# Performance work log

Measured on AMD Instinct MI355X. Metric: run time of the kernel, lower is better.

## Reference

```python
import jax, jax.numpy as jnp
import numpy as np

N_NODES = 100000
N_EDGES = 1600000
IN_CH = 64
HEADS = 8
OUT_CH = 16
NEG_SLOPE = 0.2  # PyG GATConv default


def setup_inputs() -> dict:
    key = jax.random.key(0)
    ks = jax.random.split(key, 6)
    x = jax.random.normal(ks[0], (N_NODES, IN_CH), dtype=jnp.float32)
    edge_index = jax.random.randint(ks[1], (2, N_EDGES), 0, N_NODES, dtype=jnp.int32)
    # learned parameters (PyG GATConv: shared lin for src/dst, att vectors, bias for concat output)
    W = jax.random.normal(ks[2], (HEADS * OUT_CH, IN_CH), dtype=jnp.float32) / np.sqrt(IN_CH)
    att_src = jax.random.normal(ks[3], (HEADS, OUT_CH), dtype=jnp.float32) / np.sqrt(OUT_CH)
    att_dst = jax.random.normal(ks[4], (HEADS, OUT_CH), dtype=jnp.float32) / np.sqrt(OUT_CH)
    bias = jax.random.normal(ks[5], (HEADS * OUT_CH,), dtype=jnp.float32) * 0.01
    return {"x": x, "edge_index": edge_index, "W": W,
            "att_src": att_src, "att_dst": att_dst, "bias": bias}


def reference(x, edge_index, W, att_src, att_dst, bias):
    n = x.shape[0]
    # linear projection -> [N, H, C]
    h = (x @ W.T).reshape(n, HEADS, OUT_CH)
    # per-node halves of the attention logit
    a_src = jnp.einsum('nhc,hc->nh', h, att_src)  # [N, H]
    a_dst = jnp.einsum('nhc,hc->nh', h, att_dst)  # [N, H]
    # add self loops (PyG default add_self_loops=True)
    loops = jnp.arange(n, dtype=edge_index.dtype)
    src = jnp.concatenate([edge_index[0], loops])
    dst = jnp.concatenate([edge_index[1], loops])
    # edge attention: leaky_relu then segment-softmax over incoming edges of dst
    e = jax.nn.leaky_relu(a_src[src] + a_dst[dst], NEG_SLOPE)  # [E+N, H]
    e_max = jax.ops.segment_max(e, dst, num_segments=n)
    e = jnp.exp(e - e_max[dst])
    denom = jax.ops.segment_sum(e, dst, num_segments=n)
    alpha = e / (denom[dst] + 1e-16)  # [E+N, H]
    # weighted scatter-add aggregation
    msg = h[src] * alpha[:, :, None]  # [E+N, H, C]
    out = jax.ops.segment_sum(msg, dst, num_segments=n).reshape(n, HEADS * OUT_CH)
    out = out + bias
    # unlinear: act='relu', norm=None
    return jax.nn.relu(out)
```

## Files before the change

kernel.cpp:

```cpp
#include <hip/hip_runtime.h>

#define N_NODESC 100000
#define N_EDGESC 1600000
#define HCC 128
#define E_TOTC (N_EDGESC + N_NODESC)
#define SCAN_NB 391
#define PROJ_NB 782

__device__ __forceinline__ float lrelu(float v) { return fmaxf(v, 0.2f * v); }
__device__ __forceinline__ unsigned short f2bf(float f) {
    unsigned u = __float_as_uint(f);
    unsigned r = ((u >> 16) & 1u) + 0x7fffu;
    return (unsigned short)((u + r) >> 16);
}

__global__ void wu_kernel(const float* __restrict__ W,
                          const float* __restrict__ att_src, const float* __restrict__ att_dst,
                          float* __restrict__ WT, float* __restrict__ us_g) {
    int t = blockIdx.x * 256 + threadIdx.x;
    if (t < 8192) {
        int k = t >> 7, c = t & 127;
        WT[t] = W[c * 64 + k];
    } else {
        int o = t - 8192;
        int k = o >> 4, c = o & 15;
        const int h = (c < 8) ? c : c - 8;
        const float* av = (c < 8) ? att_src : att_dst;
        float s = 0.f;
#pragma unroll
        for (int j = 0; j < 16; ++j) s += av[h * 16 + j] * W[(h * 16 + j) * 64 + k];
        us_g[o] = s;
    }
}

__launch_bounds__(256, 2)
__global__ void proj_kernel(const float* __restrict__ x, const float* __restrict__ WT,
                            const float* __restrict__ us_g,
                            unsigned short* __restrict__ h16,
                            float* __restrict__ a_src, float* __restrict__ a_dst) {
    __shared__ float xs[128][68];
    __shared__ float ws[64][132];
    __shared__ float us[64][16];
    const int t = threadIdx.x;
    const int row0 = blockIdx.x * 128;

    const float4* wt4 = (const float4*)WT;
    float4* ws4 = (float4*)&ws[0][0];
#pragma unroll
    for (int j = 0; j < 8; ++j) {
        int q = t + 256 * j;
        int k = q >> 5, c4 = q & 31;
        *(float4*)&ws[k][c4 * 4] = wt4[q];
    }
    ((float4*)&us[0][0])[t] = ((const float4*)us_g)[t];

#pragma unroll
    for (int j = 0; j < 8; ++j) {
        int f = (t + 256 * j) * 4;
        int r = f >> 6, k = f & 63;
        int gr = row0 + r;
        if (gr >= N_NODESC) gr = N_NODESC - 1;
        float4 v = *(const float4*)&x[(size_t)gr * 64 + k];
        *(float4*)&xs[r][k] = v;
    }
    __syncthreads();

    const int rg = t & 15;
    const int cg = t >> 4;
    float acc[8][8], acca[8];
#pragma unroll
    for (int i = 0; i < 8; ++i) {
        acca[i] = 0.f;
#pragma unroll
        for (int j = 0; j < 8; ++j) acc[i][j] = 0.f;
    }

#pragma unroll 4
    for (int k = 0; k < 64; ++k) {
        float xv[8];
#pragma unroll
        for (int i = 0; i < 8; ++i) xv[i] = xs[rg + 16 * i][k];
        float4 w0 = *(const float4*)&ws[k][4 * cg];
        float4 w1 = *(const float4*)&ws[k][64 + 4 * cg];
        float uv = us[k][cg];
#pragma unroll
        for (int i = 0; i < 8; ++i) {
            acc[i][0] += xv[i] * w0.x; acc[i][1] += xv[i] * w0.y;
            acc[i][2] += xv[i] * w0.z; acc[i][3] += xv[i] * w0.w;
            acc[i][4] += xv[i] * w1.x; acc[i][5] += xv[i] * w1.y;
            acc[i][6] += xv[i] * w1.z; acc[i][7] += xv[i] * w1.w;
            acca[i]   += xv[i] * uv;
        }
    }

#pragma unroll
    for (int i = 0; i < 8; ++i) {
        int gr = row0 + rg + 16 * i;
        if (gr < N_NODESC) {
            ushort4 p0, p1;
            p0.x = f2bf(acc[i][0]); p0.y = f2bf(acc[i][1]); p0.z = f2bf(acc[i][2]); p0.w = f2bf(acc[i][3]);
            p1.x = f2bf(acc[i][4]); p1.y = f2bf(acc[i][5]); p1.z = f2bf(acc[i][6]); p1.w = f2bf(acc[i][7]);
            *(ushort4*)&h16[(size_t)gr * HCC + 4 * cg] = p0;
            *(ushort4*)&h16[(size_t)gr * HCC + 64 + 4 * cg] = p1;
            if (cg < 8) a_src[(size_t)gr * 8 + cg] = acca[i];
            else        a_dst[(size_t)gr * 8 + cg - 8] = acca[i];
        }
    }
}

__global__ void pos_kernel(const int* __restrict__ ei, int* __restrict__ deg,
                           int* __restrict__ posb) {
    int e = blockIdx.x * 256 + threadIdx.x;
    if (e >= E_TOTC) return;
    int d = (e < N_EDGESC) ? ei[N_EDGESC + e] : (e - N_EDGESC);
    posb[e] = atomicAdd(&deg[d], 1);
}

__global__ void scan1_kernel(const int* __restrict__ deg, int* __restrict__ bsum) {
    __shared__ int lds[256];
    int i = blockIdx.x * 256 + threadIdx.x;
    lds[threadIdx.x] = (i < N_NODESC) ? deg[i] : 0;
    __syncthreads();
    for (int off = 128; off > 0; off >>= 1) {
        if (threadIdx.x < off) lds[threadIdx.x] += lds[threadIdx.x + off];
        __syncthreads();
    }
    if (threadIdx.x == 0) bsum[blockIdx.x] = lds[0];
}

__global__ void scan2_kernel(int* __restrict__ bsum) {
    __shared__ int lds[512];
    int t = threadIdx.x;
    lds[t] = (t < SCAN_NB) ? bsum[t] : 0;
    __syncthreads();
    for (int off = 1; off < 512; off <<= 1) {
        int u = 0;
        if (t >= off) u = lds[t - off];
        __syncthreads();
        if (t >= off) lds[t] += u;
        __syncthreads();
    }
    if (t < SCAN_NB) bsum[t] = (t == 0) ? 0 : lds[t - 1];
}

__global__ void scan3_kernel(const int* __restrict__ deg, const int* __restrict__ bsum,
                             int* __restrict__ rowptr) {
    __shared__ int lds[256];
    int t = threadIdx.x;
    int i = blockIdx.x * 256 + t;
    int v = (i < N_NODESC) ? deg[i] : 0;
    lds[t] = v;
    __syncthreads();
    for (int off = 1; off < 256; off <<= 1) {
        int u = 0;
        if (t >= off) u = lds[t - off];
        __syncthreads();
        if (t >= off) lds[t] += u;
        __syncthreads();
    }
    int excl = bsum[blockIdx.x] + lds[t] - v;
    if (i < N_NODESC) rowptr[i] = excl;
    if (i == 0) rowptr[N_NODESC] = E_TOTC;
}

__global__ void scatter_kernel(const int* __restrict__ ei, const int* __restrict__ rowptr,
                               const int* __restrict__ posb, int* __restrict__ colsrc) {
    int e = blockIdx.x * 256 + threadIdx.x;
    if (e >= E_TOTC) return;
    int s, d;
    if (e < N_EDGESC) { s = ei[e]; d = ei[N_EDGESC + e]; }
    else              { s = d = e - N_EDGESC; }
    colsrc[rowptr[d] + posb[e]] = s;
}

__launch_bounds__(256, 8)
__global__ void agg_csr_kernel(const int* __restrict__ rowptr, const int* __restrict__ colsrc,
                               const float* __restrict__ a_src, const float* __restrict__ a_dst,
                               const unsigned* __restrict__ h32,
                               const float* __restrict__ bias, float* __restrict__ out) {
    const int t = threadIdx.x;
    const int L = t & 63;
    const int n = blockIdx.x * 4 + (t >> 6);
    const int hd = L >> 3;
    const int eL = L & 7;

    const int beg = rowptr[n], end = rowptr[n + 1];
    const float ad = a_dst[n * 8 + hd];

    float den = 0.f;
    float acc[16];
#pragma unroll
    for (int j = 0; j < 16; ++j) acc[j] = 0.f;

    int p = beg + eL;
    bool vld = p < end;
    int s = vld ? colsrc[p] : 0;
    float av = vld ? a_src[s * 8 + hd] : 0.f;

    while (vld) {
        const uint4* hp = (const uint4*)(h32 + (size_t)s * 64 + hd * 8);
        const uint4 ha = hp[0];
        const uint4 hb = hp[1];
        const int p2 = p + 8;
        const bool v2 = p2 < end;
        const int s2 = v2 ? colsrc[p2] : 0;
        const float av2 = v2 ? a_src[s2 * 8 + hd] : 0.f;

        const float pr = __expf(lrelu(av + ad));
        den += pr;
        acc[0]  = fmaf(pr, __uint_as_float(ha.x << 16),         acc[0]);
        acc[1]  = fmaf(pr, __uint_as_float(ha.x & 0xffff0000u), acc[1]);
        acc[2]  = fmaf(pr, __uint_as_float(ha.y << 16),         acc[2]);
        acc[3]  = fmaf(pr, __uint_as_float(ha.y & 0xffff0000u), acc[3]);
        acc[4]  = fmaf(pr, __uint_as_float(ha.z << 16),         acc[4]);
        acc[5]  = fmaf(pr, __uint_as_float(ha.z & 0xffff0000u), acc[5]);
        acc[6]  = fmaf(pr, __uint_as_float(ha.w << 16),         acc[6]);
        acc[7]  = fmaf(pr, __uint_as_float(ha.w & 0xffff0000u), acc[7]);
        acc[8]  = fmaf(pr, __uint_as_float(hb.x << 16),         acc[8]);
        acc[9]  = fmaf(pr, __uint_as_float(hb.x & 0xffff0000u), acc[9]);
        acc[10] = fmaf(pr, __uint_as_float(hb.y << 16),         acc[10]);
        acc[11] = fmaf(pr, __uint_as_float(hb.y & 0xffff0000u), acc[11]);
        acc[12] = fmaf(pr, __uint_as_float(hb.z << 16),         acc[12]);
        acc[13] = fmaf(pr, __uint_as_float(hb.z & 0xffff0000u), acc[13]);
        acc[14] = fmaf(pr, __uint_as_float(hb.w << 16),         acc[14]);
        acc[15] = fmaf(pr, __uint_as_float(hb.w & 0xffff0000u), acc[15]);

        p = p2; s = s2; av = av2; vld = v2;
    }

    den += __shfl_xor(den, 1); den += __shfl_xor(den, 2); den += __shfl_xor(den, 4);
#pragma unroll
    for (int j = 0; j < 16; ++j) {
        acc[j] += __shfl_xor(acc[j], 1);
        acc[j] += __shfl_xor(acc[j], 2);
        acc[j] += __shfl_xor(acc[j], 4);
    }
    const float inv = 1.f / (den + 1e-16f);
    float ox = acc[0], oy = acc[1];
#pragma unroll
    for (int j = 1; j < 8; ++j) {
        ox = (eL == j) ? acc[2 * j]     : ox;
        oy = (eL == j) ? acc[2 * j + 1] : oy;
    }
    const float2 b = ((const float2*)bias)[L];
    float2 o;
    o.x = fmaxf(ox * inv + b.x, 0.f);
    o.y = fmaxf(oy * inv + b.y, 0.f);
    ((float2*)out)[(size_t)n * 64 + L] = o;
}

extern "C" void kernel_launch(void* const* d_in, const int* in_sizes, int n_in,
                              void* d_out, int out_size, void* d_ws, size_t ws_size,
                              hipStream_t stream) {
    const float* x       = (const float*)d_in[0];
    const int*   ei      = (const int*)d_in[1];
    const float* W       = (const float*)d_in[2];
    const float* att_src = (const float*)d_in[3];
    const float* att_dst = (const float*)d_in[4];
    const float* bias    = (const float*)d_in[5];
    float* out = (float*)d_out;

    float* ws    = (float*)d_ws;
    unsigned short* h16 = (unsigned short*)ws;
    float* a_src = ws + 6400000;
    float* a_dst = a_src + 800000;
    float* WT    = a_dst + 800000;
    float* us_g  = WT + 8192;
    int* deg     = (int*)(us_g + 1024);
    int* rowptr  = deg + 100000;
    int* bsum    = rowptr + 100001;
    int* posb    = bsum + 512;
    int* colsrc  = posb + 1700000;

    hipMemsetAsync(deg, 0, 100000 * sizeof(int), stream);

    wu_kernel<<<36, 256, 0, stream>>>(W, att_src, att_dst, WT, us_g);
    proj_kernel<<<PROJ_NB, 256, 0, stream>>>(x, WT, us_g, h16, a_src, a_dst);
    pos_kernel<<<(E_TOTC + 255) / 256, 256, 0, stream>>>(ei, deg, posb);
    scan1_kernel<<<SCAN_NB, 256, 0, stream>>>(deg, bsum);
    scan2_kernel<<<1, 512, 0, stream>>>(bsum);
    scan3_kernel<<<SCAN_NB, 256, 0, stream>>>(deg, bsum, rowptr);
    scatter_kernel<<<(E_TOTC + 255) / 256, 256, 0, stream>>>(ei, rowptr, posb, colsrc);

    agg_csr_kernel<<<N_NODESC / 4, 256, 0, stream>>>(rowptr, colsrc, a_src, a_dst,
                                                     (const unsigned*)h16, bias, out);
}
```

Measured before the change: 230.2 us.

## Fuse setup kernels, use single-pass decoupled-lookback scan, persistent aggregation

Merges the weight-transpose kernel with the degree/position atomic kernel, collapses the three-kernel scan into one decoupled-lookback scan with flag-tagged block states, and turns the CSR aggregation into a persistent kernel that pulls four nodes at a time from an atomic counter and prefetches their first neighbours. The aim is to cut launch count and inter-kernel bubbles and to improve load balance and latency hiding in the gather. The lookback scan relies on blocks making forward progress in order, and the persistent loop adds atomic-counter contention.

```diff
diff --git a/kernel.cpp b/kernel.cpp
--- a/kernel.cpp
+++ b/kernel.cpp
@@ -6,6 +6,12 @@
 #define E_TOTC (N_EDGESC + N_NODESC)
 #define SCAN_NB 391
 #define PROJ_NB 782
+#define POS_NB 6641
+#define WU_NB 36
+
+#define FLAG_AGG 0x40000000u
+#define FLAG_PRE 0x80000000u
+#define VAL_MASK 0x3fffffffu
 
 __device__ __forceinline__ float lrelu(float v) { return fmaxf(v, 0.2f * v); }
 __device__ __forceinline__ unsigned short f2bf(float f) {
@@ -14,23 +20,32 @@
     return (unsigned short)((u + r) >> 16);
 }
 
-__global__ void wu_kernel(const float* __restrict__ W,
-                          const float* __restrict__ att_src, const float* __restrict__ att_dst,
-                          float* __restrict__ WT, float* __restrict__ us_g) {
-    int t = blockIdx.x * 256 + threadIdx.x;
-    if (t < 8192) {
-        int k = t >> 7, c = t & 127;
-        WT[t] = W[c * 64 + k];
-    } else {
-        int o = t - 8192;
-        int k = o >> 4, c = o & 15;
-        const int h = (c < 8) ? c : c - 8;
-        const float* av = (c < 8) ? att_src : att_dst;
-        float s = 0.f;
-#pragma unroll
-        for (int j = 0; j < 16; ++j) s += av[h * 16 + j] * W[(h * 16 + j) * 64 + k];
-        us_g[o] = s;
-    }
+__global__ void wu_pos_kernel(const float* __restrict__ W,
+                              const float* __restrict__ att_src, const float* __restrict__ att_dst,
+                              float* __restrict__ WT, float* __restrict__ us_g,
+                              const int* __restrict__ ei, int* __restrict__ deg,
+                              int* __restrict__ posb) {
+    if (blockIdx.x < WU_NB) {
+        int t = blockIdx.x * 256 + threadIdx.x;
+        if (t < 8192) {
+            int k = t >> 7, c = t & 127;
+            WT[t] = W[c * 64 + k];
+        } else if (t < 9216) {
+            int o = t - 8192;
+            int k = o >> 4, c = o & 15;
+            const int h = (c < 8) ? c : c - 8;
+            const float* av = (c < 8) ? att_src : att_dst;
+            float s = 0.f;
+#pragma unroll
+            for (int j = 0; j < 16; ++j) s += av[h * 16 + j] * W[(h * 16 + j) * 64 + k];
+            us_g[o] = s;
+        }
+        return;
+    }
+    int e = (blockIdx.x - WU_NB) * 256 + threadIdx.x;
+    if (e >= E_TOTC) return;
+    int d = (e < N_EDGESC) ? ei[N_EDGESC + e] : (e - N_EDGESC);
+    posb[e] = atomicAdd(&deg[d], 1);
 }
 
 __launch_bounds__(256, 2)
@@ -45,7 +60,6 @@
     const int row0 = blockIdx.x * 128;
 
     const float4* wt4 = (const float4*)WT;
-    float4* ws4 = (float4*)&ws[0][0];
 #pragma unroll
     for (int j = 0; j < 8; ++j) {
         int q = t + 256 * j;
@@ -108,47 +122,13 @@
     }
 }
 
-__global__ void pos_kernel(const int* __restrict__ ei, int* __restrict__ deg,
-                           int* __restrict__ posb) {
-    int e = blockIdx.x * 256 + threadIdx.x;
-    if (e >= E_TOTC) return;
-    int d = (e < N_EDGESC) ? ei[N_EDGESC + e] : (e - N_EDGESC);
-    posb[e] = atomicAdd(&deg[d], 1);
-}
-
-__global__ void scan1_kernel(const int* __restrict__ deg, int* __restrict__ bsum) {
+__global__ void scan_kernel(const int* __restrict__ deg, unsigned* __restrict__ state,
+                            int* __restrict__ rowptr) {
     __shared__ int lds[256];
-    int i = blockIdx.x * 256 + threadIdx.x;
-    lds[threadIdx.x] = (i < N_NODESC) ? deg[i] : 0;
-    __syncthreads();
-    for (int off = 128; off > 0; off >>= 1) {
-        if (threadIdx.x < off) lds[threadIdx.x] += lds[threadIdx.x + off];
-        __syncthreads();
-    }
-    if (threadIdx.x == 0) bsum[blockIdx.x] = lds[0];
-}
-
-__global__ void scan2_kernel(int* __restrict__ bsum) {
-    __shared__ int lds[512];
-    int t = threadIdx.x;
-    lds[t] = (t < SCAN_NB) ? bsum[t] : 0;
-    __syncthreads();
-    for (int off = 1; off < 512; off <<= 1) {
-        int u = 0;
-        if (t >= off) u = lds[t - off];
-        __syncthreads();
-        if (t >= off) lds[t] += u;
-        __syncthreads();
-    }
-    if (t < SCAN_NB) bsum[t] = (t == 0) ? 0 : lds[t - 1];
-}
-
-__global__ void scan3_kernel(const int* __restrict__ deg, const int* __restrict__ bsum,
-                             int* __restrict__ rowptr) {
-    __shared__ int lds[256];
-    int t = threadIdx.x;
-    int i = blockIdx.x * 256 + t;
-    int v = (i < N_NODESC) ? deg[i] : 0;
+    __shared__ int s_prefix;
+    const int b = blockIdx.x, t = threadIdx.x;
+    const int i = b * 256 + t;
+    const int v = (i < N_NODESC) ? deg[i] : 0;
     lds[t] = v;
     __syncthreads();
     for (int off = 1; off < 256; off <<= 1) {
@@ -158,9 +138,28 @@
         if (t >= off) lds[t] += u;
         __syncthreads();
     }
-    int excl = bsum[blockIdx.x] + lds[t] - v;
-    if (i < N_NODESC) rowptr[i] = excl;
-    if (i == 0) rowptr[N_NODESC] = E_TOTC;
+    const int incl = lds[t];
+    const int total = lds[255];
+    if (t == 0) {
+        if (b == 0) {
+            atomicExch(&state[0], FLAG_PRE | (unsigned)total);
+            s_prefix = 0;
+        } else {
+            atomicExch(&state[b], FLAG_AGG | (unsigned)total);
+            unsigned run = 0;
+            int j = b - 1;
+            while (true) {
+                unsigned s = atomicAdd(&state[j], 0u);
+                if (s & FLAG_PRE) { run += s & VAL_MASK; break; }
+                if (s & FLAG_AGG) { run += s & VAL_MASK; --j; }
+            }
+            atomicExch(&state[b], FLAG_PRE | ((unsigned)total + run));
+            s_prefix = (int)run;
+        }
+    }
+    __syncthreads();
+    const int excl = s_prefix + incl - v;
+    if (i <= N_NODESC) rowptr[i] = excl;
 }
 
 __global__ void scatter_kernel(const int* __restrict__ ei, const int* __restrict__ rowptr,
@@ -174,79 +173,105 @@
 }
 
 __launch_bounds__(256, 8)
-__global__ void agg_csr_kernel(const int* __restrict__ rowptr, const int* __restrict__ colsrc,
-                               const float* __restrict__ a_src, const float* __restrict__ a_dst,
-                               const unsigned* __restrict__ h32,
-                               const float* __restrict__ bias, float* __restrict__ out) {
+__global__ void agg_pers_kernel(const int* __restrict__ rowptr, const int* __restrict__ colsrc,
+                                const float* __restrict__ a_src, const float* __restrict__ a_dst,
+                                const unsigned* __restrict__ h32,
+                                const float* __restrict__ bias, float* __restrict__ out,
+                                int* __restrict__ ctr) {
     const int t = threadIdx.x;
     const int L = t & 63;
-    const int n = blockIdx.x * 4 + (t >> 6);
     const int hd = L >> 3;
     const int eL = L & 7;
-
-    const int beg = rowptr[n], end = rowptr[n + 1];
-    const float ad = a_dst[n * 8 + hd];
-
-    float den = 0.f;
-    float acc[16];
-#pragma unroll
-    for (int j = 0; j < 16; ++j) acc[j] = 0.f;
-
-    int p = beg + eL;
-    bool vld = p < end;
-    int s = vld ? colsrc[p] : 0;
-    float av = vld ? a_src[s * 8 + hd] : 0.f;
-
-    while (vld) {
-        const uint4* hp = (const uint4*)(h32 + (size_t)s * 64 + hd * 8);
-        const uint4 ha = hp[0];
-        const uint4 hb = hp[1];
-        const int p2 = p + 8;
-        const bool v2 = p2 < end;
-        const int s2 = v2 ? colsrc[p2] : 0;
-        const float av2 = v2 ? a_src[s2 * 8 + hd] : 0.f;
-
-        const float pr = __expf(lrelu(av + ad));
-        den += pr;
-        acc[0]  = fmaf(pr, __uint_as_float(ha.x << 16),         acc[0]);
-        acc[1]  = fmaf(pr, __uint_as_float(ha.x & 0xffff0000u), acc[1]);
-        acc[2]  = fmaf(pr, __uint_as_float(ha.y << 16),         acc[2]);
-        acc[3]  = fmaf(pr, __uint_as_float(ha.y & 0xffff0000u), acc[3]);
-        acc[4]  = fmaf(pr, __uint_as_float(ha.z << 16),         acc[4]);
-        acc[5]  = fmaf(pr, __uint_as_float(ha.z & 0xffff0000u), acc[5]);
-        acc[6]  = fmaf(pr, __uint_as_float(ha.w << 16),         acc[6]);
-        acc[7]  = fmaf(pr, __uint_as_float(ha.w & 0xffff0000u), acc[7]);
-        acc[8]  = fmaf(pr, __uint_as_float(hb.x << 16),         acc[8]);
-        acc[9]  = fmaf(pr, __uint_as_float(hb.x & 0xffff0000u), acc[9]);
-        acc[10] = fmaf(pr, __uint_as_float(hb.y << 16),         acc[10]);
-        acc[11] = fmaf(pr, __uint_as_float(hb.y & 0xffff0000u), acc[11]);
-        acc[12] = fmaf(pr, __uint_as_float(hb.z << 16),         acc[12]);
-        acc[13] = fmaf(pr, __uint_as_float(hb.z & 0xffff0000u), acc[13]);
-        acc[14] = fmaf(pr, __uint_as_float(hb.w << 16),         acc[14]);
-        acc[15] = fmaf(pr, __uint_as_float(hb.w & 0xffff0000u), acc[15]);
-
-        p = p2; s = s2; av = av2; vld = v2;
-    }
-
-    den += __shfl_xor(den, 1); den += __shfl_xor(den, 2); den += __shfl_xor(den, 4);
-#pragma unroll
-    for (int j = 0; j < 16; ++j) {
-        acc[j] += __shfl_xor(acc[j], 1);
-        acc[j] += __shfl_xor(acc[j], 2);
-        acc[j] += __shfl_xor(acc[j], 4);
-    }
-    const float inv = 1.f / (den + 1e-16f);
-    float ox = acc[0], oy = acc[1];
-#pragma unroll
-    for (int j = 1; j < 8; ++j) {
-        ox = (eL == j) ? acc[2 * j]     : ox;
-        oy = (eL == j) ? acc[2 * j + 1] : oy;
-    }
-    const float2 b = ((const float2*)bias)[L];
-    float2 o;
-    o.x = fmaxf(ox * inv + b.x, 0.f);
-    o.y = fmaxf(oy * inv + b.y, 0.f);
-    ((float2*)out)[(size_t)n * 64 + L] = o;
+    const float2 b2 = ((const float2*)bias)[L];
+
+    while (true) {
+        int base = 0;
+        if (L == 0) base = atomicAdd(ctr, 4);
+        base = __shfl(base, 0);
+        if (base >= N_NODESC) return;
+
+        const int rv = rowptr[min(base + (L & 7), N_NODESC)];
+        const float adv = a_dst[min(base * 8 + L, N_NODESC * 8 - 1)];
+
+        int s0[4];
+        float av0[4];
+#pragma unroll
+        for (int j = 0; j < 4; ++j) {
+            int bj = __shfl(rv, j);
+            s0[j] = colsrc[min(bj + eL, E_TOTC - 1)];
+        }
+#pragma unroll
+        for (int j = 0; j < 4; ++j) av0[j] = a_src[s0[j] * 8 + hd];
+
+#pragma unroll
+        for (int j = 0; j < 4; ++j) {
+            const int n = base + j;
+            if (n >= N_NODESC) break;
+            const int beg = __shfl(rv, j);
+            const int end = __shfl(rv, j + 1);
+            const float ad = __shfl(adv, j * 8 + hd);
+
+            float den = 0.f;
+            float acc[16];
+#pragma unroll
+            for (int q = 0; q < 16; ++q) acc[q] = 0.f;
+
+            int p = beg + eL;
+            bool vld = p < end;
+            int s = s0[j];
+            float av = av0[j];
+
+            while (vld) {
+                const uint4* hp = (const uint4*)(h32 + (size_t)s * 64 + hd * 8);
+                const uint4 ha = hp[0];
+                const uint4 hb = hp[1];
+                const int p2 = p + 8;
+                const bool v2 = p2 < end;
+                const int s2 = v2 ? colsrc[p2] : 0;
+                const float av2 = v2 ? a_src[s2 * 8 + hd] : 0.f;
+
+                const float pr = __expf(lrelu(av + ad));
+                den += pr;
+                acc[0]  = fmaf(pr, __uint_as_float(ha.x << 16),         acc[0]);
+                acc[1]  = fmaf(pr, __uint_as_float(ha.x & 0xffff0000u), acc[1]);
+                acc[2]  = fmaf(pr, __uint_as_float(ha.y << 16),         acc[2]);
+                acc[3]  = fmaf(pr, __uint_as_float(ha.y & 0xffff0000u), acc[3]);
+                acc[4]  = fmaf(pr, __uint_as_float(ha.z << 16),         acc[4]);
+                acc[5]  = fmaf(pr, __uint_as_float(ha.z & 0xffff0000u), acc[5]);
+                acc[6]  = fmaf(pr, __uint_as_float(ha.w << 16),         acc[6]);
+                acc[7]  = fmaf(pr, __uint_as_float(ha.w & 0xffff0000u), acc[7]);
+                acc[8]  = fmaf(pr, __uint_as_float(hb.x << 16),         acc[8]);
+                acc[9]  = fmaf(pr, __uint_as_float(hb.x & 0xffff0000u), acc[9]);
+                acc[10] = fmaf(pr, __uint_as_float(hb.y << 16),         acc[10]);
+                acc[11] = fmaf(pr, __uint_as_float(hb.y & 0xffff0000u), acc[11]);
+                acc[12] = fmaf(pr, __uint_as_float(hb.z << 16),         acc[12]);
+                acc[13] = fmaf(pr, __uint_as_float(hb.z & 0xffff0000u), acc[13]);
+                acc[14] = fmaf(pr, __uint_as_float(hb.w << 16),         acc[14]);
+                acc[15] = fmaf(pr, __uint_as_float(hb.w & 0xffff0000u), acc[15]);
+
+                p = p2; s = s2; av = av2; vld = v2;
+            }
+
+            den += __shfl_xor(den, 1); den += __shfl_xor(den, 2); den += __shfl_xor(den, 4);
+#pragma unroll
+            for (int q = 0; q < 16; ++q) {
+                acc[q] += __shfl_xor(acc[q], 1);
+                acc[q] += __shfl_xor(acc[q], 2);
+                acc[q] += __shfl_xor(acc[q], 4);
+            }
+            const float inv = 1.f / (den + 1e-16f);
+            float ox = acc[0], oy = acc[1];
+#pragma unroll
+            for (int q = 1; q < 8; ++q) {
+                ox = (eL == q) ? acc[2 * q]     : ox;
+                oy = (eL == q) ? acc[2 * q + 1] : oy;
+            }
+            float2 o;
+            o.x = fmaxf(ox * inv + b2.x, 0.f);
+            o.y = fmaxf(oy * inv + b2.y, 0.f);
+            ((float2*)out)[(size_t)n * 64 + L] = o;
+        }
+    }
 }
 
 extern "C" void kernel_launch(void* const* d_in, const int* in_sizes, int n_in,
@@ -267,21 +292,19 @@
     float* WT    = a_dst + 800000;
     float* us_g  = WT + 8192;
     int* deg     = (int*)(us_g + 1024);
-    int* rowptr  = deg + 100000;
-    int* bsum    = rowptr + 100001;
-    int* posb    = bsum + 512;
+    unsigned* state = (unsigned*)(deg + 100000);
+    int* ctr     = (int*)(state + 392);
+    int* rowptr  = ctr + 8;
+    int* posb    = rowptr + 100001;
     int* colsrc  = posb + 1700000;
 
-    hipMemsetAsync(deg, 0, 100000 * sizeof(int), stream);
-
-    wu_kernel<<<36, 256, 0, stream>>>(W, att_src, att_dst, WT, us_g);
+    hipMemsetAsync(deg, 0, (100000 + 392 + 8) * sizeof(int), stream);
+
+    wu_pos_kernel<<<WU_NB + POS_NB, 256, 0, stream>>>(W, att_src, att_dst, WT, us_g,
+                                                      ei, deg, posb);
     proj_kernel<<<PROJ_NB, 256, 0, stream>>>(x, WT, us_g, h16, a_src, a_dst);
-    pos_kernel<<<(E_TOTC + 255) / 256, 256, 0, stream>>>(ei, deg, posb);
-    scan1_kernel<<<SCAN_NB, 256, 0, stream>>>(deg, bsum);
-    scan2_kernel<<<1, 512, 0, stream>>>(bsum);
-    scan3_kernel<<<SCAN_NB, 256, 0, stream>>>(deg, bsum, rowptr);
+    scan_kernel<<<SCAN_NB, 256, 0, stream>>>(deg, state, rowptr);
     scatter_kernel<<<(E_TOTC + 255) / 256, 256, 0, stream>>>(ei, rowptr, posb, colsrc);
-
-    agg_csr_kernel<<<N_NODESC / 4, 256, 0, stream>>>(rowptr, colsrc, a_src, a_dst,
-                                                     (const unsigned*)h16, bias, out);
-}
+    agg_pers_kernel<<<2048, 256, 0, stream>>>(rowptr, colsrc, a_src, a_dst,
+                                              (const unsigned*)h16, bias, out, ctr);
+}
```

New measurement: 562.4 us. 2.44x slower.
